# Performance work log

Measured on AMD Instinct MI355X. Metric: run time of the kernel, lower is better.

Reference implementation:

```python
import jax, jax.numpy as jnp
import numpy as np

EMBED_DIM = 1024
NUM_HEADS = 16
HEAD_DIM = EMBED_DIM // NUM_HEADS
N_PATCHES = 220
ROPE_BASE = 10000.0
EPS = 1e-6


def rms_norm(x, g):
    # x: [..., d]
    rms = jnp.sqrt(jnp.mean(x * x, axis=-1, keepdims=True) + EPS)
    return g * (x / rms)


def apply_rope(x):
    # torchtune-style interleaved RoPE. x: [b, s, h, d]
    b, s, h, d = x.shape
    theta = 1.0 / (ROPE_BASE ** (jnp.arange(0, d, 2, dtype=jnp.float32) / d))  # [d/2]
    ang = jnp.arange(s, dtype=jnp.float32)[:, None] * theta[None, :]           # [s, d/2]
    cos = jnp.cos(ang)[None, :, None, :]
    sin = jnp.sin(ang)[None, :, None, :]
    xs = x.reshape(b, s, h, d // 2, 2)
    x0, x1 = xs[..., 0], xs[..., 1]
    out = jnp.stack([x0 * cos - x1 * sin, x1 * cos + x0 * sin], axis=-1)
    return out.reshape(b, s, h, d).astype(x.dtype)


def attention_block(x, w_qkv, w_proj, b_proj, q_gain, k_gain):
    # x: [N, S, C]; one SDPA branch (shared by spatial & temporal paths)
    N, S, C = x.shape
    H, D = NUM_HEADS, HEAD_DIM
    qkv = jnp.einsum('nsc,ec->nse', x, w_qkv).reshape(N, S, 3, H, D)
    q, k, v = qkv[:, :, 0], qkv[:, :, 1], qkv[:, :, 2]  # [N, S, H, D]
    q = apply_rope(rms_norm(q, q_gain))
    k = apply_rope(rms_norm(k, k_gain))
    scale = 1.0 / jnp.sqrt(jnp.float32(D))
    scores = jnp.einsum('nqhd,nkhd->nhqk', q, k) * scale
    attn = jax.nn.softmax(scores, axis=-1)
    out = jnp.einsum('nhqk,nkhd->nqhd', attn, v).reshape(N, S, C)
    return jnp.einsum('nsc,ec->nse', out, w_proj) + b_proj


def setup_inputs() -> dict:
    key = jax.random.key(0)
    ks = jax.random.split(key, 8)
    E = EMBED_DIM
    sd = 1.0 / np.sqrt(E)
    x = jax.random.normal(ks[0], (4, 5280, E), dtype=jnp.float32)
    w_sqkv = jax.random.uniform(ks[1], (3 * E, E), jnp.float32, -sd, sd)
    w_sproj = jax.random.uniform(ks[2], (E, E), jnp.float32, -sd, sd)
    b_sproj = jax.random.uniform(ks[3], (E,), jnp.float32, -sd, sd)
    w_tqkv = jax.random.uniform(ks[4], (3 * E, E), jnp.float32, -sd, sd)
    w_tproj = jax.random.uniform(ks[5], (E, E), jnp.float32, -sd, sd)
    b_tproj = jax.random.uniform(ks[6], (E,), jnp.float32, -sd, sd)
    g = jnp.ones((HEAD_DIM,), jnp.float32)
    return {
        'x': x,
        'w_sqkv': w_sqkv, 'w_sproj': w_sproj, 'b_sproj': b_sproj,
        'w_tqkv': w_tqkv, 'w_tproj': w_tproj, 'b_tproj': b_tproj,
        'sq_gain': g, 'sk_gain': g, 'tq_gain': g, 'tk_gain': g,
    }


def reference(x, w_sqkv, w_sproj, b_sproj, w_tqkv, w_tproj, b_tproj,
              sq_gain, sk_gain, tq_gain, tk_gain):
    B, T, C = x.shape
    P = N_PATCHES
    F = T // P
    # spatial attention per frame: (b f) p c
    xs = x.reshape(B, F, P, C).reshape(B * F, P, C)
    out_s = attention_block(xs, w_sqkv, w_sproj, b_sproj, sq_gain, sk_gain)
    # temporal attention per patch: (b p) f c
    xt = out_s.reshape(B, F, P, C).transpose(0, 2, 1, 3).reshape(B * P, F, C)
    out_t = attention_block(xt, w_tqkv, w_tproj, b_tproj, tq_gain, tk_gain)
    # (b p) f c -> b (f p) c
    out = out_t.reshape(B, P, F, C).transpose(0, 2, 1, 3).reshape(B, F * P, C)
    return out
```

## Files before the change

### kernel.cpp

```cpp
#include <hip/hip_runtime.h>

typedef _Float16 f16;
typedef _Float16 f16x8 __attribute__((ext_vector_type(8)));
typedef f16x8 f16x8a __attribute__((may_alias));
typedef float f32x4 __attribute__((ext_vector_type(4)));

#define NTOK 21120
#define MPAD 21248
#define SCALE_Q 0.18033688f

__device__ __forceinline__ void gll16(const void* g, void* l) {
  __builtin_amdgcn_global_load_lds(
      (const __attribute__((address_space(1))) unsigned int*)g,
      (__attribute__((address_space(3))) unsigned int*)l, 16, 0, 0);
}

__device__ __forceinline__ unsigned int pack2(float a, float b) {
  union { f16 h[2]; unsigned int u; } c;
  c.h[0] = (f16)a; c.h[1] = (f16)b;
  return c.u;
}
__device__ __forceinline__ unsigned short f2h(float a) {
  union { f16 h; unsigned short u; } c; c.h = (f16)a; return c.u;
}

template <int C>
__device__ __forceinline__ float dppf(float x) {
  union { float f; int i; } u, r;
  u.f = x;
  r.i = __builtin_amdgcn_update_dpp(0, u.i, C, 0xf, 0xf, true);
  return r.f;
}

__global__ __launch_bounds__(256) void cast_kernel(
    const float* __restrict__ in, unsigned short* __restrict__ out, int n4) {
  int i = blockIdx.x * 256 + threadIdx.x;
  if (i >= n4) return;
  float4 v = ((const float4*)in)[i];
  uint2 o;
  o.x = pack2(v.x, v.y);
  o.y = pack2(v.z, v.w);
  ((uint2*)out)[i] = o;
}

__global__ __launch_bounds__(256) void transpose_cast_kernel(
    const float* __restrict__ in, unsigned short* __restrict__ out) {
  __shared__ float tile[32][33];
  int bx = blockIdx.x & 31, by = blockIdx.x >> 5;
  int tx = threadIdx.x & 31, ty = threadIdx.x >> 5;
#pragma unroll
  for (int i = 0; i < 32; i += 8)
    tile[ty + i][tx] = in[(size_t)(by * 32 + ty + i) * 1024 + bx * 32 + tx];
  __syncthreads();
#pragma unroll
  for (int i = 0; i < 32; i += 8)
    out[(size_t)(bx * 32 + ty + i) * 1024 + by * 32 + tx] = f2h(tile[tx][ty + i]);
}

__global__ __launch_bounds__(256) void bias_combine_kernel(
    const float* __restrict__ w, const float* __restrict__ b, float* __restrict__ bc) {
  int e = blockIdx.x * 256 + threadIdx.x;
  if (e >= 3072) return;
  const float4* wr = (const float4*)(w + (size_t)e * 1024);
  const float4* b4 = (const float4*)b;
  float s = 0.f;
  for (int c = 0; c < 256; ++c) {
    float4 wv = wr[c], bv = b4[c];
    s += wv.x * bv.x + wv.y * bv.y + wv.z * bv.z + wv.w * bv.w;
  }
  bc[e] = s;
}

__global__ __launch_bounds__(256) void rope_table_kernel(float2* tabS, float2* tabT) {
  int t = blockIdx.x * 256 + threadIdx.x;
  const float lb = logf(10000.0f) * (1.0f / 32.0f);
  if (t < 220 * 32) {
    int s = t >> 5, i = t & 31;
    float theta = expf(-(float)i * lb);
    float ang = (float)s * theta;
    tabS[t] = make_float2(cosf(ang), sinf(ang));
  } else if (t < 220 * 32 + 24 * 32) {
    int u = t - 220 * 32;
    int s = u >> 5, i = u & 31;
    float theta = expf(-(float)i * lb);
    float ang = (float)s * theta;
    tabT[u] = make_float2(cosf(ang), sinf(ang));
  }
}

__global__ __launch_bounds__(256) void gemm_bt(
    const unsigned short* __restrict__ A, const unsigned short* __restrict__ B,
    const float* __restrict__ bias, void* __restrict__ C,
    int M, int N, int K, int outmode,
    const float2* __restrict__ tab, const float* __restrict__ gq,
    const float* __restrict__ gk, int mode) {
  __shared__ __align__(16) unsigned short sh[16384];
  unsigned short* As = sh;
  unsigned short* Bs = sh + 8192;
  const int tid = threadIdx.x;
  const int w = tid >> 6, lane = tid & 63;
  const int l15 = lane & 15, quad = lane >> 4;
  const int wr = w >> 1, wc = w & 1;

  const int ntn = N >> 7;
  const int stride = ntn << 3;
  const int g = blockIdx.x / stride, r = blockIdx.x % stride;
  const int tn = r % ntn, tm = g * 8 + r / ntn;

  f32x4 acc[4][4];
#pragma unroll
  for (int a = 0; a < 4; ++a)
#pragma unroll
    for (int b = 0; b < 4; ++b) acc[a][b] = (f32x4){0.f, 0.f, 0.f, 0.f};

  const int srow = tid >> 3;
  const int schk = tid & 7;
  const size_t arow0 = (size_t)tm * 128;
  const size_t brow0 = (size_t)tn * 128;
  const int nk = K >> 6;

  for (int kt = 0; kt < nk; ++kt) {
    __syncthreads();
    const int kb = kt << 6;
#pragma unroll
    for (int rd = 0; rd < 4; ++rd) {
      int row = rd * 32 + srow;
      int sc = (schk ^ (row & 7)) * 8;
      gll16(A + (arow0 + row) * K + kb + sc, (char*)As + rd * 4096 + tid * 16);
      gll16(B + (brow0 + row) * K + kb + sc, (char*)Bs + rd * 4096 + tid * 16);
    }
    __syncthreads();
#pragma unroll
    for (int kk = 0; kk < 2; ++kk) {
      f16x8 af[4], bf[4];
#pragma unroll
      for (int mt = 0; mt < 4; ++mt) {
        int ra = wr * 64 + mt * 16 + l15;
        af[mt] = *(const f16x8a*)((const char*)As + ra * 128 + (((kk * 4 + quad) ^ (ra & 7)) * 16));
        int rb = wc * 64 + mt * 16 + l15;
        bf[mt] = *(const f16x8a*)((const char*)Bs + rb * 128 + (((kk * 4 + quad) ^ (rb & 7)) * 16));
      }
#pragma unroll
      for (int mt = 0; mt < 4; ++mt)
#pragma unroll
        for (int nt = 0; nt < 4; ++nt)
          acc[mt][nt] = __builtin_amdgcn_mfma_f32_16x16x32_f16(af[mt], bf[nt], acc[mt][nt], 0, 0, 0);
    }
  }

  unsigned short* Cs = (unsigned short*)C;
#pragma unroll
  for (int p = 0; p < 2; ++p) {
    __syncthreads();
#pragma unroll
    for (int mi = 0; mi < 2; ++mi) {
      int mt = p * 2 + mi;
      int rl = wr * 32 + mi * 16 + quad * 4;
#pragma unroll
      for (int nt = 0; nt < 4; ++nt) {
        int cl = wc * 64 + nt * 16 + l15;
#pragma unroll
        for (int rg = 0; rg < 4; ++rg)
          sh[(rl + rg) * 136 + cl] = f2h(acc[mt][nt][rg]);
      }
    }
    __syncthreads();
#pragma unroll
    for (int c = 0; c < 4; ++c) {
      int rl = c * 16 + (tid >> 4), cx = tid & 15;
      int grow = tm * 128 + ((rl >> 5) << 6) + p * 32 + (rl & 31);
      uint4 v = *(const uint4*)&sh[rl * 136 + cx * 8];
      *(uint4*)&Cs[(size_t)grow * N + tn * 128 + cx * 8] = v;
    }
  }
}

#define FENCE() asm volatile("" ::: "memory")
#define BAR() do { FENCE(); __builtin_amdgcn_s_barrier(); FENCE(); } while (0)
#define WAITV(N) asm volatile("s_waitcnt vmcnt(" #N ")" ::: "memory")
#define ASLOT(T) (((T) % 3) * 32768)
#define BSLOT(T) (98304 + ((T) & 1) * 32768)
#define LDAf(T, mt, kk) (*(const f16x8a*)(smem + ASLOT(T) + wrOff + (mt) * 2048 + (aoff ^ ((kk) << 6))))
#define LDBf(T, nt, kk) (*(const f16x8a*)(smem + BSLOT(T) + bcOff + (nt) * 2048 + (aoff ^ ((kk) << 6))))
#define STAGE_A2(T, h) do { \
    gll16(aSp + (size_t)((h) * 128) * K + (T) * 64, smem + ASLOT(T) + (h) * 16384 + tid * 16); \
    gll16(aSp + (size_t)((h) * 128 + 64) * K + (T) * 64, smem + ASLOT(T) + (h) * 16384 + 8192 + tid * 16); \
  } while (0)
#define STAGE_B2(T, h) do { \
    gll16(bSp + (size_t)((h) * 128) * K + (T) * 64, smem + BSLOT(T) + (h) * 16384 + tid * 16); \
    gll16(bSp + (size_t)((h) * 128 + 64) * K + (T) * 64, smem + BSLOT(T) + (h) * 16384 + 8192 + tid * 16); \
  } while (0)
#define MM16(QB, A0_, A1_, A2_, A3_, B0_, B1_, B2_, B3_) do { \
    acc[QB + 0][0] = __builtin_amdgcn_mfma_f32_16x16x32_f16(A0_, B0_, acc[QB + 0][0], 0, 0, 0); \
    acc[QB + 0][1] = __builtin_amdgcn_mfma_f32_16x16x32_f16(A0_, B1_, acc[QB + 0][1], 0, 0, 0); \
    acc[QB + 0][2] = __builtin_amdgcn_mfma_f32_16x16x32_f16(A0_, B2_, acc[QB + 0][2], 0, 0, 0); \
    acc[QB + 0][3] = __builtin_amdgcn_mfma_f32_16x16x32_f16(A0_, B3_, acc[QB + 0][3], 0, 0, 0); \
    acc[QB + 1][0] = __builtin_amdgcn_mfma_f32_16x16x32_f16(A1_, B0_, acc[QB + 1][0], 0, 0, 0); \
    acc[QB + 1][1] = __builtin_amdgcn_mfma_f32_16x16x32_f16(A1_, B1_, acc[QB + 1][1], 0, 0, 0); \
    acc[QB + 1][2] = __builtin_amdgcn_mfma_f32_16x16x32_f16(A1_, B2_, acc[QB + 1][2], 0, 0, 0); \
    acc[QB + 1][3] = __builtin_amdgcn_mfma_f32_16x16x32_f16(A1_, B3_, acc[QB + 1][3], 0, 0, 0); \
    acc[QB + 2][0] = __builtin_amdgcn_mfma_f32_16x16x32_f16(A2_, B0_, acc[QB + 2][0], 0, 0, 0); \
    acc[QB + 2][1] = __builtin_amdgcn_mfma_f32_16x16x32_f16(A2_, B1_, acc[QB + 2][1], 0, 0, 0); \
    acc[QB + 2][2] = __builtin_amdgcn_mfma_f32_16x16x32_f16(A2_, B2_, acc[QB + 2][2], 0, 0, 0); \
    acc[QB + 2][3] = __builtin_amdgcn_mfma_f32_16x16x32_f16(A2_, B3_, acc[QB + 2][3], 0, 0, 0); \
    acc[QB + 3][0] = __builtin_amdgcn_mfma_f32_16x16x32_f16(A3_, B0_, acc[QB + 3][0], 0, 0, 0); \
    acc[QB + 3][1] = __builtin_amdgcn_mfma_f32_16x16x32_f16(A3_, B1_, acc[QB + 3][1], 0, 0, 0); \
    acc[QB + 3][2] = __builtin_amdgcn_mfma_f32_16x16x32_f16(A3_, B2_, acc[QB + 3][2], 0, 0, 0); \
    acc[QB + 3][3] = __builtin_amdgcn_mfma_f32_16x16x32_f16(A3_, B3_, acc[QB + 3][3], 0, 0, 0); \
  } while (0)

__global__ __launch_bounds__(512, 2) void gemm256(
    const unsigned short* __restrict__ A, const unsigned short* __restrict__ B,
    const float* __restrict__ bias, void* __restrict__ C,
    int M, int N, int K, int outmode,
    const float2* __restrict__ tab, const float* __restrict__ gq,
    const float* __restrict__ gk, int mode) {
  extern __shared__ char smem[];
  const int tid = threadIdx.x;
  const int w = tid >> 6, lane = tid & 63;
  const int l15 = lane & 15, quad = lane >> 4;
  const int wr = w >> 2, wc = w & 3;

  const int nwg = gridDim.x;
  const int qd = nwg >> 3, rm = nwg & 7;
  const int xcd = blockIdx.x & 7, lin = blockIdx.x >> 3;
  const int wgid = (xcd < rm ? xcd * (qd + 1) : rm * (qd + 1) + (xcd - rm) * qd) + lin;
  const int ntn = N >> 8;
  const int stg = ntn << 3;
  const int g = wgid / stg, r2 = wgid % stg;
  const int tn = r2 % ntn, tm = g * 8 + r2 / ntn;

  const int wrOff = wr * 16384;
  const int bcOff = (wc >> 1) * 16384 + (wc & 1) * 8192;
  const int aoff = l15 * 128 + ((quad ^ (l15 & 7)) << 4);

  const int sc = ((tid & 7) ^ ((tid >> 3) & 7)) * 8;
  const unsigned short* aSp = A + (size_t)(tm * 256 + (tid >> 3)) * K + sc;
  const unsigned short* bSp = B + (size_t)(tn * 256 + (tid >> 3)) * K + sc;

  f32x4 acc[8][4];
#pragma unroll
  for (int i = 0; i < 8; ++i)
#pragma unroll
    for (int j = 0; j < 4; ++j) acc[i][j] = (f32x4){0.f, 0.f, 0.f, 0.f};

  STAGE_A2(0, 0); STAGE_A2(0, 1);
  STAGE_B2(0, 0); STAGE_B2(0, 1);
  STAGE_A2(1, 0); STAGE_A2(1, 1);
  WAITV(4);
  BAR();

#pragma unroll
  for (int t = 0; t < 16; ++t) {
    f16x8 a0, a1, a2, a3, b0, b1, b2, b3;
    b0 = LDBf(t, 0, 0); b1 = LDBf(t, 1, 0); b2 = LDBf(t, 2, 0); b3 = LDBf(t, 3, 0);
    a0 = LDAf(t, 0, 0); a1 = LDAf(t, 1, 0); a2 = LDAf(t, 2, 0); a3 = LDAf(t, 3, 0);
    if (t <= 14) STAGE_B2(t + 1, 0);
    BAR();
    __builtin_amdgcn_s_setprio(1);
    MM16(0, a0, a1, a2, a3, b0, b1, b2, b3);
    __builtin_amdgcn_s_setprio(0);
    BAR();
    a0 = LDAf(t, 4, 0); a1 = LDAf(t, 5, 0); a2 = LDAf(t, 6, 0); a3 = LDAf(t, 7, 0);
    if (t <= 14) STAGE_B2(t + 1, 1);
    BAR();
    __builtin_amdgcn_s_setprio(1);
    MM16(4, a0, a1, a2, a3, b0, b1, b2, b3);
    __builtin_amdgcn_s_setprio(0);
    BAR();
    b0 = LDBf(t, 0, 1); b1 = LDBf(t, 1, 1); b2 = LDBf(t, 2, 1); b3 = LDBf(t, 3, 1);
    a0 = LDAf(t, 0, 1); a1 = LDAf(t, 1, 1); a2 = LDAf(t, 2, 1); a3 = LDAf(t, 3, 1);
    if (t <= 13) STAGE_A2(t + 2, 0);
    BAR();
    __builtin_amdgcn_s_setprio(1);
    MM16(0, a0, a1, a2, a3, b0, b1, b2, b3);
    __builtin_amdgcn_s_setprio(0);
    BAR();
    a0 = LDAf(t, 4, 1); a1 = LDAf(t, 5, 1); a2 = LDAf(t, 6, 1); a3 = LDAf(t, 7, 1);
    if (t <= 13) STAGE_A2(t + 2, 1);
    BAR();
    __builtin_amdgcn_s_setprio(1);
    MM16(4, a0, a1, a2, a3, b0, b1, b2, b3);
    __builtin_amdgcn_s_setprio(0);
    if (t <= 13) { WAITV(4); } else if (t == 14) { WAITV(0); }
    BAR();
  }

  BAR();
  const size_t grow0 = (size_t)tm * 256 + wr * 128;
  const int gcol0 = tn * 256 + wc * 64;

  float bl[4] = {0.f, 0.f, 0.f, 0.f};
  if (bias != nullptr) {
#pragma unroll
    for (int nt = 0; nt < 4; ++nt) bl[nt] = bias[gcol0 + nt * 16 + l15];
  }

  if (outmode == 2) {
    float* wf = (float*)(smem + w * 16384);
    const int frow = lane >> 4, fc = lane & 15;
#pragma unroll
    for (int h = 0; h < 2; ++h) {
#pragma unroll
      for (int mi = 0; mi < 4; ++mi)
#pragma unroll
        for (int nt = 0; nt < 4; ++nt)
#pragma unroll
          for (int rg = 0; rg < 4; ++rg) {
            int row = mi * 16 + quad * 4 + rg;
            int col = nt * 16 + l15;
            int c = col >> 2, lo = col & 3;
            wf[row * 64 + ((c ^ (row & 15)) << 2) + lo] = acc[h * 4 + mi][nt][rg] + bl[nt];
          }
#pragma unroll
      for (int it = 0; it < 16; ++it) {
        int row = it * 4 + frow;
        float4 v = *(const float4*)(wf + row * 64 + ((fc ^ (row & 15)) << 2));
        size_t gr = grow0 + h * 64 + row;
        if (gr < (size_t)M)
          *(float4*)((float*)C + gr * N + gcol0 + fc * 4) = v;
      }
    }
    return;
  }

  unsigned short* wh = (unsigned short*)(smem + w * 16384);
  if (outmode == 3 && tn < 8) {
    const int isQ = tn < 4;
    const float* gg = isQ ? gq : gk;
    float gv[4];
#pragma unroll
    for (int nt = 0; nt < 4; ++nt) gv[nt] = gg[nt * 16 + l15];
#pragma unroll
    for (int mt = 0; mt < 8; ++mt) {
      float v[4][4], rr[4];
#pragma unroll
      for (int rg = 0; rg < 4; ++rg) rr[rg] = 0.f;
#pragma unroll
      for (int nt = 0; nt < 4; ++nt)
#pragma unroll
        for (int rg = 0; rg < 4; ++rg) {
          float x = acc[mt][nt][rg] + bl[nt];
          v[nt][rg] = x;
          rr[rg] += x * x;
        }
#pragma unroll
      for (int rg = 0; rg < 4; ++rg) {
        float s = rr[rg];
        s += dppf<0xB1>(s);
        s += dppf<0x4E>(s);
        s += dppf<0x141>(s);
        s += dppf<0x140>(s);
        float r = rsqrtf(s * (1.0f / 64.0f) + 1e-6f);
        rr[rg] = isQ ? r * SCALE_Q : r;
      }
      int pos[4];
#pragma unroll
      for (int rg = 0; rg < 4; ++rg) {
        int grow = (int)grow0 + mt * 16 + quad * 4 + rg;
        pos[rg] = mode ? ((grow / 220) % 24) : (grow % 220);
      }
#pragma unroll
      for (int nt = 0; nt < 4; ++nt) {
        int col = nt * 16 + l15;
        int ii = nt * 8 + (l15 >> 1);
        int c = col >> 3, lo = col & 7;
#pragma unroll
        for (int rg = 0; rg < 4; ++rg) {
          float2 cs = tab[pos[rg] * 32 + ii];
          float x = v[nt][rg] * rr[rg] * gv[nt];
          float p = dppf<0xB1>(x);
          float o = (l15 & 1) ? (x * cs.x + p * cs.y) : (x * cs.x - p * cs.y);
          int row = mt * 16 + quad * 4 + rg;
          wh[row * 64 + ((c ^ (row & 7)) << 3) + lo] = f2h(o);
        }
      }
    }
  } else {
#pragma unroll
    for (int mt = 0; mt < 8; ++mt)
#pragma unroll
      for (int nt = 0; nt < 4; ++nt) {
        int col = nt * 16 + l15;
        int c = col >> 3, lo = col & 7;
#pragma unroll
        for (int rg = 0; rg < 4; ++rg) {
          int row = mt * 16 + quad * 4 + rg;
          wh[row * 64 + ((c ^ (row & 7)) << 3) + lo] = f2h(acc[mt][nt][rg] + bl[nt]);
        }
      }
  }
  {
    const int frow = lane >> 3, fch = lane & 7;
    unsigned short* C16 = (unsigned short*)C;
#pragma unroll
    for (int it = 0; it < 16; ++it) {
      int row = it * 8 + frow;
      uint4 vv = *(const uint4*)((const char*)wh + row * 128 + ((fch ^ (row & 7)) << 4));
      size_t gr = grow0 + row;
      if (gr < (size_t)M)
        *(uint4*)(C16 + gr * N + gcol0 + fch * 8) = vv;
    }
  }
}

__global__ __launch_bounds__(256) void attn_spatial(
    const unsigned short* __restrict__ qkv, unsigned short* __restrict__ aout) {
  __shared__ __align__(16) unsigned short sh[30720];
  unsigned short* Kls = sh;
  unsigned short* Vt = sh + 8192;
  unsigned short* P = sh + 22528;
  const int tid = threadIdx.x;
  const int w = tid >> 6, lane = tid & 63;
  const int l15 = lane & 15, quad = lane >> 4;
  const int n = blockIdx.x >> 4, h = blockIdx.x & 15;
  const size_t tb = (size_t)n * 220;
  const unsigned short* qbase = qkv + tb * 3072 + h * 64;

  f16x8 aq[4][2];
#pragma unroll
  for (int mt = 0; mt < 4; ++mt) {
    int row = w * 64 + mt * 16 + l15;
    if (row > 219) row = 219;
#pragma unroll
    for (int c = 0; c < 2; ++c)
      aq[mt][c] = *(const f16x8a*)(qbase + (size_t)row * 3072 + c * 32 + quad * 8);
  }
  if (tid < 220) {
    const uint4* src = (const uint4*)(qbase + (size_t)tid * 3072 + 2048);
    uint4 vv[8];
#pragma unroll
    for (int c = 0; c < 8; ++c) vv[c] = src[c];
    const unsigned short* us = (const unsigned short*)vv;
#pragma unroll
    for (int d = 0; d < 64; ++d) Vt[d * 224 + tid] = us[d];
  } else if (tid < 224) {
#pragma unroll
    for (int d = 0; d < 64; ++d) Vt[d * 224 + tid] = 0;
  }

  float lsum[4][4];
  f32x4 o[4][4];
#pragma unroll
  for (int mt = 0; mt < 4; ++mt)
#pragma unroll
    for (int rg = 0; rg < 4; ++rg) lsum[mt][rg] = 0.f;
#pragma unroll
  for (int mt = 0; mt < 4; ++mt)
#pragma unroll
    for (int nt = 0; nt < 4; ++nt) o[mt][nt] = (f32x4){0.f, 0.f, 0.f, 0.f};

  const int xr = (l15 & 3) ^ ((l15 >> 2) & 3);
  unsigned short* Pw = P + w * 2048;

  for (int half = 0; half < 2; ++half) {
    const int k0 = half * 128;
    const int nslot = half ? 736 : 1024;
#pragma unroll
    for (int k = 0; k < 4; ++k) {
      int slot = k * 256 + tid;
      if (slot < nslot) {
        int rl = slot >> 3, c = slot & 7;
        gll16(qbase + (size_t)(k0 + rl) * 3072 + 1024 + ((c ^ (rl & 7)) * 8),
              (char*)Kls + k * 4096 + w * 1024);
      }
    }
    __syncthreads();
    const int nci = half ? 3 : 4;
    for (int ci = 0; ci < nci; ++ci) {
      const int cig = half * 4 + ci;
      f16x8 bk[2][2];
#pragma unroll
      for (int ct = 0; ct < 2; ++ct) {
        int rl = ci * 32 + ct * 16 + l15;
#pragma unroll
        for (int c = 0; c < 2; ++c)
          bk[ct][c] = *(const f16x8a*)((const char*)Kls + rl * 128 + (((quad + 4 * c) ^ (rl & 7)) * 16));
      }
      f32x4 sc[4][2];
#pragma unroll
      for (int mt = 0; mt < 4; ++mt)
#pragma unroll
        for (int ct = 0; ct < 2; ++ct) {
          f32x4 z = (f32x4){0.f, 0.f, 0.f, 0.f};
          z = __builtin_amdgcn_mfma_f32_16x16x32_f16(aq[mt][0], bk[ct][0], z, 0, 0, 0);
          sc[mt][ct] = __builtin_amdgcn_mfma_f32_16x16x32_f16(aq[mt][1], bk[ct][1], z, 0, 0, 0);
        }
      const int okk = (cig * 32 + 16 + l15) < 220;
#pragma unroll
      for (int mt = 0; mt < 4; ++mt)
#pragma unroll
        for (int rg = 0; rg < 4; ++rg) {
          float p0 = exp2f(sc[mt][0][rg]);
          float p1 = okk ? exp2f(sc[mt][1][rg]) : 0.0f;
          lsum[mt][rg] += p0 + p1;
          int xw = quad ^ rg;
          unsigned short* pb = Pw + (mt * 16 + quad * 4 + rg) * 32;
          pb[(((l15 >> 3) ^ xw) * 8) + (l15 & 7)] = f2h(p0);
          pb[(((2 + (l15 >> 3)) ^ xw) * 8) + (l15 & 7)] = f2h(p1);
        }
      __asm__ volatile("s_waitcnt lgkmcnt(0)" ::: "memory");
      f16x8 ap[4], bv[4];
#pragma unroll
      for (int mt = 0; mt < 4; ++mt)
        ap[mt] = *(const f16x8a*)((const char*)Pw + (mt * 16 + l15) * 64 + (quad ^ xr) * 16);
#pragma unroll
      for (int nt = 0; nt < 4; ++nt)
        bv[nt] = *(const f16x8a*)((const char*)Vt + (nt * 16 + l15) * 448 + cig * 64 + quad * 16);
#pragma unroll
      for (int mt = 0; mt < 4; ++mt)
#pragma unroll
        for (int nt = 0; nt < 4; ++nt)
          o[mt][nt] = __builtin_amdgcn_mfma_f32_16x16x32_f16(ap[mt], bv[nt], o[mt][nt], 0, 0, 0);
    }
    __syncthreads();
  }

#pragma unroll
  for (int mt = 0; mt < 4; ++mt)
#pragma unroll
    for (int rg = 0; rg < 4; ++rg) {
      float l = lsum[mt][rg];
      l += __shfl_xor(l, 1);
      l += __shfl_xor(l, 2);
      l += __shfl_xor(l, 4);
      l += __shfl_xor(l, 8);
      int s = w * 64 + mt * 16 + quad * 4 + rg;
      if (s < 220) {
        float inv = 1.0f / l;
        unsigned short* dst = aout + (tb + s) * 1024 + h * 64;
#pragma unroll
        for (int nt = 0; nt < 4; ++nt) dst[nt * 16 + l15] = f2h(o[mt][nt][rg] * inv);
      }
    }
}

__global__ __launch_bounds__(256) void attn_temporal(
    const unsigned short* __restrict__ qkv, unsigned short* __restrict__ aout) {
  __shared__ __align__(16) unsigned short sh[14336];
  const int tid = threadIdx.x;
  const int w = tid >> 6, lane = tid & 63;
  const int l15 = lane & 15, quad = lane >> 4;
  const int b = blockIdx.x / 880;
  const int rem = blockIdx.x % 880;
  const int p = rem >> 2, hq = rem & 3;
  const int h = hq * 4 + w;
  unsigned short* Vtw = sh + w * 2560;
  unsigned short* Pw = sh + 10240 + w * 1024;
  const unsigned short* base = qkv + ((size_t)(b * 24) * 220 + p) * 3072 + h * 64;
  const size_t fs = (size_t)220 * 3072;

  {
    int r = lane >> 1, hf = lane & 1;
    if (r < 24) {
      const uint4* src = (const uint4*)(base + r * fs + 2048 + hf * 32);
      uint4 vv[4];
#pragma unroll
      for (int c = 0; c < 4; ++c) vv[c] = src[c];
      const unsigned short* us = (const unsigned short*)vv;
#pragma unroll
      for (int j = 0; j < 32; ++j) Vtw[(hf * 32 + j) * 40 + r] = us[j];
    } else {
#pragma unroll
      for (int j = 0; j < 32; ++j) Vtw[(hf * 32 + j) * 40 + r] = 0;
    }
  }
  f16x8 aq[2][2], bk[2][2];
#pragma unroll
  for (int mt = 0; mt < 2; ++mt) {
    int row = mt * 16 + l15;
    if (row > 23) row = 23;
#pragma unroll
    for (int c = 0; c < 2; ++c)
      aq[mt][c] = *(const f16x8a*)(base + row * fs + c * 32 + quad * 8);
  }
#pragma unroll
  for (int ct = 0; ct < 2; ++ct) {
    int row = ct * 16 + l15;
    if (row > 23) row = 23;
#pragma unroll
    for (int c = 0; c < 2; ++c)
      bk[ct][c] = *(const f16x8a*)(base + row * fs + 1024 + c * 32 + quad * 8);
  }
  f32x4 sc[2][2];
#pragma unroll
  for (int mt = 0; mt < 2; ++mt)
#pragma unroll
    for (int ct = 0; ct < 2; ++ct) {
      f32x4 z = (f32x4){0.f, 0.f, 0.f, 0.f};
      z = __builtin_amdgcn_mfma_f32_16x16x32_f16(aq[mt][0], bk[ct][0], z, 0, 0, 0);
      sc[mt][ct] = __builtin_amdgcn_mfma_f32_16x16x32_f16(aq[mt][1], bk[ct][1], z, 0, 0, 0);
    }
  const int xr = (l15 & 3) ^ ((l15 >> 2) & 3);
  const int okk = l15 < 8;
  float lr[2][4];
#pragma unroll
  for (int mt = 0; mt < 2; ++mt)
#pragma unroll
    for (int rg = 0; rg < 4; ++rg) {
      float p0 = exp2f(sc[mt][0][rg]);
      float p1 = okk ? exp2f(sc[mt][1][rg]) : 0.0f;
      float rs = p0 + p1;
      rs += __shfl_xor(rs, 1);
      rs += __shfl_xor(rs, 2);
      rs += __shfl_xor(rs, 4);
      rs += __shfl_xor(rs, 8);
      lr[mt][rg] = rs;
      int xw = quad ^ rg;
      unsigned short* pb = Pw + (mt * 16 + quad * 4 + rg) * 32;
      pb[(((l15 >> 3) ^ xw) * 8) + (l15 & 7)] = f2h(p0);
      pb[(((2 + (l15 >> 3)) ^ xw) * 8) + (l15 & 7)] = f2h(p1);
    }
  __asm__ volatile("s_waitcnt lgkmcnt(0)" ::: "memory");
  f16x8 ap[2], bv[4];
#pragma unroll
  for (int mt = 0; mt < 2; ++mt)
    ap[mt] = *(const f16x8a*)((const char*)Pw + (mt * 16 + l15) * 64 + (quad ^ xr) * 16);
#pragma unroll
  for (int nt = 0; nt < 4; ++nt)
    bv[nt] = *(const f16x8a*)((const char*)Vtw + (nt * 16 + l15) * 80 + quad * 16);
  f32x4 o[2][4];
#pragma unroll
  for (int mt = 0; mt < 2; ++mt)
#pragma unroll
    for (int nt = 0; nt < 4; ++nt) {
      f32x4 z = (f32x4){0.f, 0.f, 0.f, 0.f};
      o[mt][nt] = __builtin_amdgcn_mfma_f32_16x16x32_f16(ap[mt], bv[nt], z, 0, 0, 0);
    }
#pragma unroll
  for (int mt = 0; mt < 2; ++mt)
#pragma unroll
    for (int rg = 0; rg < 4; ++rg) {
      int s = mt * 16 + quad * 4 + rg;
      if (s < 24) {
        float inv = 1.0f / lr[mt][rg];
        unsigned short* dst = aout + ((size_t)(b * 24 + s) * 220 + p) * 1024 + h * 64;
#pragma unroll
        for (int nt = 0; nt < 4; ++nt) dst[nt * 16 + l15] = f2h(o[mt][nt][rg] * inv);
      }
    }
}

extern "C" void kernel_launch(void* const* d_in, const int* in_sizes, int n_in,
                              void* d_out, int out_size, void* d_ws, size_t ws_size,
                              hipStream_t stream) {
  (void)in_sizes; (void)n_in; (void)out_size; (void)ws_size;
  const float* x = (const float*)d_in[0];
  const float* wsqkv = (const float*)d_in[1];
  const float* wsproj = (const float*)d_in[2];
  const float* bsproj = (const float*)d_in[3];
  const float* wtqkv = (const float*)d_in[4];
  const float* wtproj = (const float*)d_in[5];
  const float* btproj = (const float*)d_in[6];
  const float* sqg = (const float*)d_in[7];
  const float* skg = (const float*)d_in[8];
  const float* tqg = (const float*)d_in[9];
  const float* tkg = (const float*)d_in[10];

  static bool attr_done = false;
  if (!attr_done) {
    hipFuncSetAttribute(reinterpret_cast<const void*>(gemm256),
                        hipFuncAttributeMaxDynamicSharedMemorySize, 163840);
    attr_done = true;
  }

  char* ws = (char*)d_ws;
  size_t off = 0;
  auto alloc = [&](size_t bytes) {
    char* ptr = ws + off;
    off += (bytes + 255) & ~(size_t)255;
    return ptr;
  };
  unsigned short* xb = (unsigned short*)alloc((size_t)MPAD * 1024 * 2);
  unsigned short* qkvb = (unsigned short*)alloc((size_t)NTOK * 3072 * 2);
  unsigned short* aoutb = (unsigned short*)alloc((size_t)MPAD * 1024 * 2);
  unsigned short* wsqkvb = (unsigned short*)alloc((size_t)3072 * 1024 * 2);
  unsigned short* wsprojTb = (unsigned short*)alloc((size_t)1024 * 1024 * 2);
  unsigned short* wtqkvb = (unsigned short*)alloc((size_t)3072 * 1024 * 2);
  unsigned short* wtprojb = (unsigned short*)alloc((size_t)1024 * 1024 * 2);
  unsigned short* wcb = (unsigned short*)alloc((size_t)3072 * 1024 * 2);
  float* bcb = (float*)alloc(3072 * 4);
  float2* tabS = (float2*)alloc(220 * 32 * 8);
  float2* tabT = (float2*)alloc(24 * 32 * 8);

  hipMemsetAsync(xb + (size_t)NTOK * 1024, 0, (size_t)(MPAD - NTOK) * 1024 * 2, stream);
  hipMemsetAsync(aoutb + (size_t)NTOK * 1024, 0, (size_t)(MPAD - NTOK) * 1024 * 2, stream);

  dim3 blk(256);
  cast_kernel<<<21120, blk, 0, stream>>>(x, xb, 5406720);
  cast_kernel<<<3072, blk, 0, stream>>>(wsqkv, wsqkvb, 786432);
  cast_kernel<<<3072, blk, 0, stream>>>(wtqkv, wtqkvb, 786432);
  cast_kernel<<<1024, blk, 0, stream>>>(wtproj, wtprojb, 262144);
  transpose_cast_kernel<<<1024, blk, 0, stream>>>(wsproj, wsprojTb);
  bias_combine_kernel<<<12, blk, 0, stream>>>(wtqkv, bsproj, bcb);
  rope_table_kernel<<<31, blk, 0, stream>>>(tabS, tabT);

  gemm_bt<<<dim3(24 * 8), blk, 0, stream>>>(wtqkvb, wsprojTb, nullptr, wcb, 3072, 1024, 1024, 0,
                                            nullptr, nullptr, nullptr, 0);

  dim3 blk512(512);
  gemm256<<<dim3(83 * 12), blk512, 163840, stream>>>(xb, wsqkvb, nullptr, qkvb, NTOK, 3072, 1024, 3,
                                                     tabS, sqg, skg, 0);
  attn_spatial<<<dim3(1536), blk, 0, stream>>>(qkvb, aoutb);
  gemm256<<<dim3(83 * 12), blk512, 163840, stream>>>(aoutb, wcb, bcb, qkvb, NTOK, 3072, 1024, 3,
                                                     tabT, tqg, tkg, 1);
  attn_temporal<<<dim3(3520), blk, 0, stream>>>(qkvb, aoutb);
  gemm256<<<dim3(83 * 4), blk512, 163840, stream>>>(aoutb, wtprojb, btproj, (float*)d_out,
                                                    NTOK, 1024, 1024, 2,
                                                    nullptr, nullptr, nullptr, 0);
}
```

Baseline: 714.4 us.

## Replace per-phase barriers in GEMM main loop with LDS waitcnt software pipelining

Removes most intra-iteration workgroup barriers in the 256x256 GEMM K-loop and instead issues LDS fragment loads ahead of the MFMA groups that need them, gating them with explicit lgkmcnt waits and sched barriers. Global-to-LDS staging for the next tiles is issued in one batch per half-iteration. This aims to cut barrier stalls and overlap LDS reads with MFMA work, at the cost of more live vector registers (24 fragments) and relying on the triple/double LDS buffering to avoid overwrite hazards without barriers.

```diff
diff --git a/kernel.cpp b/kernel.cpp
--- a/kernel.cpp
+++ b/kernel.cpp
@@ -178,6 +178,8 @@
 #define FENCE() asm volatile("" ::: "memory")
 #define BAR() do { FENCE(); __builtin_amdgcn_s_barrier(); FENCE(); } while (0)
 #define WAITV(N) asm volatile("s_waitcnt vmcnt(" #N ")" ::: "memory")
+#define WAITL(N) do { asm volatile("s_waitcnt lgkmcnt(" #N ")" ::: "memory"); \
+                      __builtin_amdgcn_sched_barrier(0); } while (0)
 #define ASLOT(T) (((T) % 3) * 32768)
 #define BSLOT(T) (98304 + ((T) & 1) * 32768)
 #define LDAf(T, mt, kk) (*(const f16x8a*)(smem + ASLOT(T) + wrOff + (mt) * 2048 + (aoff ^ ((kk) << 6))))
@@ -252,41 +254,37 @@
 
 #pragma unroll
   for (int t = 0; t < 16; ++t) {
-    f16x8 a0, a1, a2, a3, b0, b1, b2, b3;
-    b0 = LDBf(t, 0, 0); b1 = LDBf(t, 1, 0); b2 = LDBf(t, 2, 0); b3 = LDBf(t, 3, 0);
-    a0 = LDAf(t, 0, 0); a1 = LDAf(t, 1, 0); a2 = LDAf(t, 2, 0); a3 = LDAf(t, 3, 0);
-    if (t <= 14) STAGE_B2(t + 1, 0);
-    BAR();
+    f16x8 bA0, bA1, bA2, bA3, bB0, bB1, bB2, bB3;
+    f16x8 aA0, aA1, aA2, aA3, aB0, aB1, aB2, aB3;
+    f16x8 aC0, aC1, aC2, aC3, aD0, aD1, aD2, aD3;
+    bA0 = LDBf(t, 0, 0); bA1 = LDBf(t, 1, 0); bA2 = LDBf(t, 2, 0); bA3 = LDBf(t, 3, 0);
+    aA0 = LDAf(t, 0, 0); aA1 = LDAf(t, 1, 0); aA2 = LDAf(t, 2, 0); aA3 = LDAf(t, 3, 0);
+    aB0 = LDAf(t, 4, 0); aB1 = LDAf(t, 5, 0); aB2 = LDAf(t, 6, 0); aB3 = LDAf(t, 7, 0);
+    if (t <= 14) { STAGE_B2(t + 1, 0); STAGE_B2(t + 1, 1); }
+    WAITL(4);
     __builtin_amdgcn_s_setprio(1);
-    MM16(0, a0, a1, a2, a3, b0, b1, b2, b3);
+    MM16(0, aA0, aA1, aA2, aA3, bA0, bA1, bA2, bA3);
     __builtin_amdgcn_s_setprio(0);
-    BAR();
-    a0 = LDAf(t, 4, 0); a1 = LDAf(t, 5, 0); a2 = LDAf(t, 6, 0); a3 = LDAf(t, 7, 0);
-    if (t <= 14) STAGE_B2(t + 1, 1);
-    BAR();
+    bB0 = LDBf(t, 0, 1); bB1 = LDBf(t, 1, 1); bB2 = LDBf(t, 2, 1); bB3 = LDBf(t, 3, 1);
+    aC0 = LDAf(t, 0, 1); aC1 = LDAf(t, 1, 1); aC2 = LDAf(t, 2, 1); aC3 = LDAf(t, 3, 1);
+    WAITL(8);
     __builtin_amdgcn_s_setprio(1);
-    MM16(4, a0, a1, a2, a3, b0, b1, b2, b3);
+    MM16(4, aB0, aB1, aB2, aB3, bA0, bA1, bA2, bA3);
     __builtin_amdgcn_s_setprio(0);
-    BAR();
-    b0 = LDBf(t, 0, 1); b1 = LDBf(t, 1, 1); b2 = LDBf(t, 2, 1); b3 = LDBf(t, 3, 1);
-    a0 = LDAf(t, 0, 1); a1 = LDAf(t, 1, 1); a2 = LDAf(t, 2, 1); a3 = LDAf(t, 3, 1);
-    if (t <= 13) STAGE_A2(t + 2, 0);
-    BAR();
+    aD0 = LDAf(t, 4, 1); aD1 = LDAf(t, 5, 1); aD2 = LDAf(t, 6, 1); aD3 = LDAf(t, 7, 1);
+    if (t <= 13) { STAGE_A2(t + 2, 0); STAGE_A2(t + 2, 1); }
+    WAITL(4);
     __builtin_amdgcn_s_setprio(1);
-    MM16(0, a0, a1, a2, a3, b0, b1, b2, b3);
+    MM16(0, aC0, aC1, aC2, aC3, bB0, bB1, bB2, bB3);
     __builtin_amdgcn_s_setprio(0);
-    BAR();
-    a0 = LDAf(t, 4, 1); a1 = LDAf(t, 5, 1); a2 = LDAf(t, 6, 1); a3 = LDAf(t, 7, 1);
-    if (t <= 13) STAGE_A2(t + 2, 1);
-    BAR();
+    WAITL(0);
     __builtin_amdgcn_s_setprio(1);
-    MM16(4, a0, a1, a2, a3, b0, b1, b2, b3);
+    MM16(4, aD0, aD1, aD2, aD3, bB0, bB1, bB2, bB3);
     __builtin_amdgcn_s_setprio(0);
     if (t <= 13) { WAITV(4); } else if (t == 14) { WAITV(0); }
     BAR();
   }
 
-  BAR();
   const size_t grow0 = (size_t)tm * 256 + wr * 128;
   const int gcol0 = tn * 256 + wc * 64;
 
```

Measured after the change: 722.5 us. No clear change (+1.1%).
